# Kernel optimization log

Hardware: AMD Instinct MI355X
Metric: run time of the kernel (lower is better)

## Reference

```python
import jax, jax.numpy as jnp
import numpy as np

SEQ_LEN = 2048

def setup_inputs() -> dict:
    key = jax.random.key(0)
    kq, kk, kv = jax.random.split(key, 3)
    B, S, D = 8, SEQ_LEN, 64
    q = jax.random.normal(kq, (B, S, D), dtype=jnp.float32)
    k = jax.random.normal(kk, (B, S, D), dtype=jnp.float32)
    v = jax.random.normal(kv, (B, S, D), dtype=jnp.float32)
    return {"q": q, "k": k, "v": v}

def reference(q, k, v):
    # scores: [B, S, S] = q @ k^T  (note: original applies NO 1/sqrt(d) scaling)
    scores = jnp.einsum('bqd,bkd->bqk', q, k)
    S = scores.shape[-1]
    causal = jnp.tril(jnp.ones((S, S), dtype=bool))  # lower-triangular mask
    scores = jnp.where(causal, scores, -jnp.inf)
    weights = jax.nn.softmax(scores, axis=-1)
    return jnp.einsum('bqk,bkd->bqd', weights, v)
```

## Files before the change

kernel.cpp:

```cpp
#include <hip/hip_runtime.h>


#define BATCH 8
#define SEQ 2048
#define DIM 64
#define NEL (BATCH * SEQ * DIM)

typedef __attribute__((ext_vector_type(8))) short short8;
typedef __attribute__((ext_vector_type(4))) float f32x4;

#define MFMA(a, b, c) __builtin_amdgcn_mfma_f32_16x16x32_bf16(a, b, c, 0, 0, 0)

__device__ __forceinline__ unsigned short f2bf(float x) {
    unsigned u = __float_as_uint(x);
    unsigned r = u + 0x7fffu + ((u >> 16) & 1u);
    return (unsigned short)(r >> 16);
}
__device__ __forceinline__ float bf2f(unsigned short h) {
    return __uint_as_float(((unsigned)h) << 16);
}
__device__ __forceinline__ short8 ld8(const unsigned short* p) {
    return *(const short8*)p;
}
__device__ __forceinline__ void splitA(float4 a, float4 b, short8& h8, short8& l8) {
    float v[8] = {a.x, a.y, a.z, a.w, b.x, b.y, b.z, b.w};
#pragma unroll
    for (int i = 0; i < 8; ++i) {
        unsigned u  = __float_as_uint(v[i]);
        unsigned hu = u & 0xffff0000u;
        h8[i] = (short)(hu >> 16);
        float lf = v[i] - __uint_as_float(hu);
        l8[i] = (short)(__float_as_uint(lf) >> 16);
    }
}

__device__ __forceinline__ float dpp_max16(float x) {
    float o;
    o = __int_as_float(__builtin_amdgcn_update_dpp(0, __float_as_int(x), 0xB1, 0xF, 0xF, true));
    x = fmaxf(x, o);
    o = __int_as_float(__builtin_amdgcn_update_dpp(0, __float_as_int(x), 0x4E, 0xF, 0xF, true));
    x = fmaxf(x, o);
    o = __int_as_float(__builtin_amdgcn_update_dpp(0, __float_as_int(x), 0x141, 0xF, 0xF, true));
    x = fmaxf(x, o);
    o = __int_as_float(__builtin_amdgcn_update_dpp(0, __float_as_int(x), 0x140, 0xF, 0xF, true));
    return fmaxf(x, o);
}
__device__ __forceinline__ float dpp_sum16(float x) {
    float o;
    o = __int_as_float(__builtin_amdgcn_update_dpp(0, __float_as_int(x), 0xB1, 0xF, 0xF, true));
    x += o;
    o = __int_as_float(__builtin_amdgcn_update_dpp(0, __float_as_int(x), 0x4E, 0xF, 0xF, true));
    x += o;
    o = __int_as_float(__builtin_amdgcn_update_dpp(0, __float_as_int(x), 0x141, 0xF, 0xF, true));
    x += o;
    o = __int_as_float(__builtin_amdgcn_update_dpp(0, __float_as_int(x), 0x140, 0xF, 0xF, true));
    return x + o;
}

__global__ __launch_bounds__(256) void prep(
    const float* __restrict__ K, const float* __restrict__ V,
    unsigned short* __restrict__ Kf, unsigned short* __restrict__ Vf)
{
    __shared__ unsigned short sT[64][72];
    const int blk = blockIdx.x;
    const int t = threadIdx.x;

    if (blk < 512) {
        const int g  = blk * 256 + t;
        const int l  = g & 63;
        const int h  = (g >> 6) & 1;
        const int Sg = g >> 7;
        const int b  = Sg >> 7;
        const int S  = Sg & 127;
        const int key = S * 16 + (l & 15);
        const float* src = K + ((size_t)(b * SEQ + key)) * DIM + h * 32 + (l >> 4) * 8;
        float4 a = *(const float4*)src;
        float4 c = *(const float4*)(src + 4);
        float v[8] = {a.x, a.y, a.z, a.w, c.x, c.y, c.z, c.w};
        short8 h8, l8;
#pragma unroll
        for (int i = 0; i < 8; ++i) {
            unsigned short hh = f2bf(v[i]);
            h8[i] = (short)hh;
            l8[i] = (short)f2bf(v[i] - bf2f(hh));
        }
        unsigned short* dst = Kf + (((size_t)Sg) << 11) + (h << 9) + l * 8;
        *(short8*)dst = h8;
        *(short8*)(dst + 1024) = l8;
        return;
    }

    const int tile = blk - 512;
    const int b = tile >> 5;
    const int s0 = (tile & 31) * 64;
    const int srow = t >> 4;
    const int d4   = (t & 15) * 4;
#pragma unroll
    for (int i = 0; i < 4; ++i) {
        const int row = srow + i * 16;
        float4 v = *(const float4*)(V + ((size_t)(b * SEQ + s0 + row)) * DIM + d4);
        sT[d4 + 0][row] = f2bf(v.x);
        sT[d4 + 1][row] = f2bf(v.y);
        sT[d4 + 2][row] = f2bf(v.z);
        sT[d4 + 3][row] = f2bf(v.w);
    }
    __syncthreads();
#pragma unroll
    for (int i = 0; i < 2; ++i) {
        const int fid = t + i * 256;
        const int cc  = fid >> 8;
        const int nt  = (fid >> 6) & 3;
        const int l   = fid & 63;
        const int key = cc * 32 + (l >> 4) * 8;
        const int dim = nt * 16 + (l & 15);
        const int c   = (s0 >> 5) + cc;
        unsigned short* dst =
            Vf + ((((size_t)(b * 64 + c)) * 4 + nt) << 9) + l * 8;
        *(float4*)dst = *(const float4*)&sT[dim][key];
    }
}

__global__ __launch_bounds__(256) void attn_main(
    const float* __restrict__ Q,
    const unsigned short* __restrict__ Kf,
    const unsigned short* __restrict__ Vf, float* __restrict__ O)
{
    __shared__ __align__(16) char scratch[4][4352];
    __shared__ float sMl[4][16][2];

    const int bid  = blockIdx.x;
    const int g    = bid >> 8;
    const int idx  = bid & 255;
    const int b    = idx & (BATCH - 1);
    const int tl   = idx >> 3;
    const int qt   = (g & 1) ? (g * 32 + 31 - tl) : (g * 32 + tl);

    const int t    = threadIdx.x;
    const int w    = t >> 6;
    const int lane = t & 63;
    const int quad = lane >> 4;
    const int n16  = lane & 15;
    const int boff = b * SEQ;

    unsigned short* sPw = (unsigned short*)scratch[w];
    float*          sOw = (float*)scratch[w];

    const unsigned short* KfL = Kf + (((size_t)(b * 128)) << 11) + lane * 8;

    const int q0 = qt * 16;
    const int q_max = q0 + 15;

    short8 qh0, ql0, qh1, ql1;
    {
        const float* qb = Q + ((size_t)(boff + q0 + n16)) * DIM + quad * 8;
        splitA(*(const float4*)(qb),      *(const float4*)(qb + 4),  qh0, ql0);
        splitA(*(const float4*)(qb + 32), *(const float4*)(qb + 36), qh1, ql1);
    }

    float m0 = -1e30f, m1 = -1e30f, m2 = -1e30f, m3 = -1e30f;
    float l0 = 0.f, l1 = 0.f, l2 = 0.f, l3 = 0.f;
    f32x4 oacc[4];
#pragma unroll
    for (int i = 0; i < 4; ++i) oacc[i] = (f32x4){0.f, 0.f, 0.f, 0.f};

    for (int kb = w * 128; kb <= q_max; kb += 512) {
        const int rem  = q_max - kb;
        const int nsub = min(8, (rem >> 4) + 1);
        const int nchain = (nsub + 1) >> 1;
        f32x4 sacc[8];

#pragma unroll
        for (int gp = 0; gp < 4; ++gp) {
            const int stA = 2 * gp, stB = stA + 1;
            if (stA < nsub) {
                const unsigned short* pA = KfL + (((size_t)((kb >> 4) + stA)) << 11);
                short8 khA0 = ld8(pA),        khA1 = ld8(pA + 512);
                short8 klA0 = ld8(pA + 1024), klA1 = ld8(pA + 1536);
                const bool okB = (stB < nsub);
                const unsigned short* pB = KfL + (((size_t)((kb >> 4) + stB)) << 11);
                short8 khB0, khB1, klB0, klB1;
                if (okB) {
                    khB0 = ld8(pB);        khB1 = ld8(pB + 512);
                    klB0 = ld8(pB + 1024); klB1 = ld8(pB + 1536);
                }
                f32x4 accA = (f32x4){0.f, 0.f, 0.f, 0.f};
                accA = MFMA(qh0, khA0, accA);
                accA = MFMA(qh1, khA1, accA);
                accA = MFMA(qh0, klA0, accA);
                accA = MFMA(qh1, klA1, accA);
                accA = MFMA(ql0, khA0, accA);
                accA = MFMA(ql1, khA1, accA);
                sacc[stA] = accA;
                if (okB) {
                    f32x4 accB = (f32x4){0.f, 0.f, 0.f, 0.f};
                    accB = MFMA(qh0, khB0, accB);
                    accB = MFMA(qh1, khB1, accB);
                    accB = MFMA(qh0, klB0, accB);
                    accB = MFMA(qh1, klB1, accB);
                    accB = MFMA(ql0, khB0, accB);
                    accB = MFMA(ql1, khB1, accB);
                    sacc[stB] = accB;
                } else {
                    sacc[stB] = (f32x4){-1e30f, -1e30f, -1e30f, -1e30f};
                }
            } else {
                sacc[stA] = (f32x4){-1e30f, -1e30f, -1e30f, -1e30f};
                sacc[stB] = (f32x4){-1e30f, -1e30f, -1e30f, -1e30f};
            }
        }

        if (kb + 127 > q0) {
#pragma unroll
            for (int st = 0; st < 8; ++st) {
                if (st < nsub) {
                    const int key = kb + st * 16 + n16;
#pragma unroll
                    for (int r = 0; r < 4; ++r)
                        if (key > q0 + quad * 4 + r) sacc[st][r] = -1e30f;
                }
            }
        }

        float mt0 = sacc[0][0], mt1 = sacc[0][1], mt2 = sacc[0][2], mt3 = sacc[0][3];
#pragma unroll
        for (int st = 1; st < 8; ++st) {
            mt0 = fmaxf(mt0, sacc[st][0]);
            mt1 = fmaxf(mt1, sacc[st][1]);
            mt2 = fmaxf(mt2, sacc[st][2]);
            mt3 = fmaxf(mt3, sacc[st][3]);
        }
        mt0 = dpp_max16(mt0); mt1 = dpp_max16(mt1);
        mt2 = dpp_max16(mt2); mt3 = dpp_max16(mt3);
        const float mn0 = fmaxf(m0, mt0), mn1 = fmaxf(m1, mt1);
        const float mn2 = fmaxf(m2, mt2), mn3 = fmaxf(m3, mt3);
        const float a0 = __expf(m0 - mn0), a1 = __expf(m1 - mn1);
        const float a2 = __expf(m2 - mn2), a3 = __expf(m3 - mn3);
        m0 = mn0; m1 = mn1; m2 = mn2; m3 = mn3;

        float ps0 = 0.f, ps1 = 0.f, ps2 = 0.f, ps3 = 0.f;
        const int stmax = 2 * nchain;
#pragma unroll
        for (int st = 0; st < 8; ++st) {
            if (st < stmax) {
                float p0 = 0.f, p1 = 0.f, p2 = 0.f, p3 = 0.f;
                if (st < nsub) {
                    p0 = __expf(sacc[st][0] - mn0);
                    p1 = __expf(sacc[st][1] - mn1);
                    p2 = __expf(sacc[st][2] - mn2);
                    p3 = __expf(sacc[st][3] - mn3);
                    ps0 += p0; ps1 += p1; ps2 += p2; ps3 += p3;
                }
                const int col = st * 16 + n16;
                sPw[(quad * 4 + 0) * 136 + col] = f2bf(p0);
                sPw[(quad * 4 + 1) * 136 + col] = f2bf(p1);
                sPw[(quad * 4 + 2) * 136 + col] = f2bf(p2);
                sPw[(quad * 4 + 3) * 136 + col] = f2bf(p3);
            }
        }
        ps0 = dpp_sum16(ps0); ps1 = dpp_sum16(ps1);
        ps2 = dpp_sum16(ps2); ps3 = dpp_sum16(ps3);
        l0 = l0 * a0 + ps0; l1 = l1 * a1 + ps1;
        l2 = l2 * a2 + ps2; l3 = l3 * a3 + ps3;
#pragma unroll
        for (int nt = 0; nt < 4; ++nt) {
            oacc[nt][0] *= a0; oacc[nt][1] *= a1;
            oacc[nt][2] *= a2; oacc[nt][3] *= a3;
        }

#pragma unroll
        for (int ch = 0; ch < 4; ++ch) {
            if (ch < nchain) {
                short8 pa = ld8(&sPw[n16 * 136 + ch * 32 + quad * 8]);
                const size_t cbase =
                    (((size_t)(b * 64 + (kb >> 5) + ch)) * 4) << 9;
#pragma unroll
                for (int nt = 0; nt < 4; ++nt) {
                    short8 vv = ld8(Vf + cbase + (nt << 9) + lane * 8);
                    oacc[nt] = MFMA(pa, vv, oacc[nt]);
                }
            }
        }
    }

#pragma unroll
    for (int nt = 0; nt < 4; ++nt)
#pragma unroll
        for (int r = 0; r < 4; ++r)
            sOw[(quad * 4 + r) * 68 + nt * 16 + n16] = oacc[nt][r];
    if (n16 == 0) {
        sMl[w][quad * 4 + 0][0] = m0; sMl[w][quad * 4 + 0][1] = l0;
        sMl[w][quad * 4 + 1][0] = m1; sMl[w][quad * 4 + 1][1] = l1;
        sMl[w][quad * 4 + 2][0] = m2; sMl[w][quad * 4 + 2][1] = l2;
        sMl[w][quad * 4 + 3][0] = m3; sMl[w][quad * 4 + 3][1] = l3;
    }
    __syncthreads();

    const int row  = t >> 4;
    const int col4 = (t & 15) * 4;
    float M = fmaxf(fmaxf(sMl[0][row][0], sMl[1][row][0]),
                    fmaxf(sMl[2][row][0], sMl[3][row][0]));
    float L = 0.f;
    float ox = 0.f, oy = 0.f, oz = 0.f, ow = 0.f;
#pragma unroll
    for (int wv = 0; wv < 4; ++wv) {
        const float ew = __expf(sMl[wv][row][0] - M);
        L += ew * sMl[wv][row][1];
        const float* op = (const float*)scratch[wv] + row * 68 + col4;
        ox += ew * op[0]; oy += ew * op[1]; oz += ew * op[2]; ow += ew * op[3];
    }
    const float inv = 1.0f / L;
    float4 res = make_float4(ox * inv, oy * inv, oz * inv, ow * inv);
    *(float4*)(O + ((size_t)(boff + q0 + row)) * DIM + col4) = res;
}

extern "C" void kernel_launch(void* const* d_in, const int* in_sizes, int n_in,
                              void* d_out, int out_size, void* d_ws, size_t ws_size,
                              hipStream_t stream) {
    const float* q = (const float*)d_in[0];
    const float* k = (const float*)d_in[1];
    const float* v = (const float*)d_in[2];
    float* out = (float*)d_out;

    unsigned short* Kf = (unsigned short*)d_ws;
    unsigned short* Vf = Kf + 2 * NEL;

    prep<<<dim3(512 + 256), dim3(256), 0, stream>>>(k, v, Kf, Vf);
    attn_main<<<dim3(1024), dim3(256), 0, stream>>>(q, Kf, Vf, out);
}
```

Baseline: 90.27 us.

## Process 32 query rows per block to reuse K and V tiles across two query subtiles

Each block now handles 32 query rows as two 16-row subtiles that share every loaded K and V fragment, and the grid is halved to 512 blocks. This cuts global K/V load traffic per query row in half and amortises address math and the softmax bookkeeping loop. In exchange, register pressure roughly doubles (two sets of score and output accumulators), shared scratch doubles, and fewer blocks means less parallelism and coarser causal load balancing, even though the tile ordering is still paired front/back.

```diff
diff --git a/kernel.cpp b/kernel.cpp
--- a/kernel.cpp
+++ b/kernel.cpp
@@ -125,15 +125,15 @@
     const unsigned short* __restrict__ Kf,
     const unsigned short* __restrict__ Vf, float* __restrict__ O)
 {
-    __shared__ __align__(16) char scratch[4][4352];
-    __shared__ float sMl[4][16][2];
+    __shared__ __align__(16) char scratch[4][8704];
+    __shared__ float sMl[4][32][2];
 
     const int bid  = blockIdx.x;
-    const int g    = bid >> 8;
+    const int gph  = bid >> 8;
     const int idx  = bid & 255;
     const int b    = idx & (BATCH - 1);
     const int tl   = idx >> 3;
-    const int qt   = (g & 1) ? (g * 32 + 31 - tl) : (g * 32 + tl);
+    const int qt   = gph ? (63 - tl) : tl;
 
     const int t    = threadIdx.x;
     const int w    = t >> 6;
@@ -147,65 +147,60 @@
 
     const unsigned short* KfL = Kf + (((size_t)(b * 128)) << 11) + lane * 8;
 
-    const int q0 = qt * 16;
-    const int q_max = q0 + 15;
-
-    short8 qh0, ql0, qh1, ql1;
+    const int q0 = qt * 32;
+    const int q_max = q0 + 31;
+
+    short8 qAh0, qAl0, qAh1, qAl1, qBh0, qBl0, qBh1, qBl1;
     {
-        const float* qb = Q + ((size_t)(boff + q0 + n16)) * DIM + quad * 8;
-        splitA(*(const float4*)(qb),      *(const float4*)(qb + 4),  qh0, ql0);
-        splitA(*(const float4*)(qb + 32), *(const float4*)(qb + 36), qh1, ql1);
+        const float* qa = Q + ((size_t)(boff + q0 + n16)) * DIM + quad * 8;
+        splitA(*(const float4*)(qa),      *(const float4*)(qa + 4),  qAh0, qAl0);
+        splitA(*(const float4*)(qa + 32), *(const float4*)(qa + 36), qAh1, qAl1);
+        const float* qb = qa + 16 * DIM;
+        splitA(*(const float4*)(qb),      *(const float4*)(qb + 4),  qBh0, qBl0);
+        splitA(*(const float4*)(qb + 32), *(const float4*)(qb + 36), qBh1, qBl1);
     }
 
     float m0 = -1e30f, m1 = -1e30f, m2 = -1e30f, m3 = -1e30f;
+    float m4 = -1e30f, m5 = -1e30f, m6 = -1e30f, m7 = -1e30f;
     float l0 = 0.f, l1 = 0.f, l2 = 0.f, l3 = 0.f;
-    f32x4 oacc[4];
-#pragma unroll
-    for (int i = 0; i < 4; ++i) oacc[i] = (f32x4){0.f, 0.f, 0.f, 0.f};
+    float l4 = 0.f, l5 = 0.f, l6 = 0.f, l7 = 0.f;
+    f32x4 oacc0[4], oacc1[4];
+#pragma unroll
+    for (int i = 0; i < 4; ++i) {
+        oacc0[i] = (f32x4){0.f, 0.f, 0.f, 0.f};
+        oacc1[i] = (f32x4){0.f, 0.f, 0.f, 0.f};
+    }
 
     for (int kb = w * 128; kb <= q_max; kb += 512) {
-        const int rem  = q_max - kb;
-        const int nsub = min(8, (rem >> 4) + 1);
+        const int nsub = min(8, ((q_max - kb) >> 4) + 1);
         const int nchain = (nsub + 1) >> 1;
-        f32x4 sacc[8];
-
-#pragma unroll
-        for (int gp = 0; gp < 4; ++gp) {
-            const int stA = 2 * gp, stB = stA + 1;
-            if (stA < nsub) {
-                const unsigned short* pA = KfL + (((size_t)((kb >> 4) + stA)) << 11);
-                short8 khA0 = ld8(pA),        khA1 = ld8(pA + 512);
-                short8 klA0 = ld8(pA + 1024), klA1 = ld8(pA + 1536);
-                const bool okB = (stB < nsub);
-                const unsigned short* pB = KfL + (((size_t)((kb >> 4) + stB)) << 11);
-                short8 khB0, khB1, klB0, klB1;
-                if (okB) {
-                    khB0 = ld8(pB);        khB1 = ld8(pB + 512);
-                    klB0 = ld8(pB + 1024); klB1 = ld8(pB + 1536);
-                }
-                f32x4 accA = (f32x4){0.f, 0.f, 0.f, 0.f};
-                accA = MFMA(qh0, khA0, accA);
-                accA = MFMA(qh1, khA1, accA);
-                accA = MFMA(qh0, klA0, accA);
-                accA = MFMA(qh1, klA1, accA);
-                accA = MFMA(ql0, khA0, accA);
-                accA = MFMA(ql1, khA1, accA);
-                sacc[stA] = accA;
-                if (okB) {
-                    f32x4 accB = (f32x4){0.f, 0.f, 0.f, 0.f};
-                    accB = MFMA(qh0, khB0, accB);
-                    accB = MFMA(qh1, khB1, accB);
-                    accB = MFMA(qh0, klB0, accB);
-                    accB = MFMA(qh1, klB1, accB);
-                    accB = MFMA(ql0, khB0, accB);
-                    accB = MFMA(ql1, khB1, accB);
-                    sacc[stB] = accB;
-                } else {
-                    sacc[stB] = (f32x4){-1e30f, -1e30f, -1e30f, -1e30f};
-                }
+        f32x4 sacc0[8], sacc1[8];
+
+#pragma unroll
+        for (int st = 0; st < 8; ++st) {
+            if (st < nsub) {
+                const unsigned short* p = KfL + (((size_t)((kb >> 4) + st)) << 11);
+                short8 kh0 = ld8(p),        kh1 = ld8(p + 512);
+                short8 kl0 = ld8(p + 1024), kl1 = ld8(p + 1536);
+                f32x4 a = (f32x4){0.f, 0.f, 0.f, 0.f};
+                a = MFMA(qAh0, kh0, a);
+                a = MFMA(qAh1, kh1, a);
+                a = MFMA(qAh0, kl0, a);
+                a = MFMA(qAh1, kl1, a);
+                a = MFMA(qAl0, kh0, a);
+                a = MFMA(qAl1, kh1, a);
+                sacc0[st] = a;
+                f32x4 c = (f32x4){0.f, 0.f, 0.f, 0.f};
+                c = MFMA(qBh0, kh0, c);
+                c = MFMA(qBh1, kh1, c);
+                c = MFMA(qBh0, kl0, c);
+                c = MFMA(qBh1, kl1, c);
+                c = MFMA(qBl0, kh0, c);
+                c = MFMA(qBl1, kh1, c);
+                sacc1[st] = c;
             } else {
-                sacc[stA] = (f32x4){-1e30f, -1e30f, -1e30f, -1e30f};
-                sacc[stB] = (f32x4){-1e30f, -1e30f, -1e30f, -1e30f};
+                sacc0[st] = (f32x4){-1e30f, -1e30f, -1e30f, -1e30f};
+                sacc1[st] = (f32x4){-1e30f, -1e30f, -1e30f, -1e30f};
             }
         }
 
@@ -215,68 +210,101 @@
                 if (st < nsub) {
                     const int key = kb + st * 16 + n16;
 #pragma unroll
-                    for (int r = 0; r < 4; ++r)
-                        if (key > q0 + quad * 4 + r) sacc[st][r] = -1e30f;
+                    for (int r = 0; r < 4; ++r) {
+                        if (key > q0 + quad * 4 + r)      sacc0[st][r] = -1e30f;
+                        if (key > q0 + 16 + quad * 4 + r) sacc1[st][r] = -1e30f;
+                    }
                 }
             }
         }
 
-        float mt0 = sacc[0][0], mt1 = sacc[0][1], mt2 = sacc[0][2], mt3 = sacc[0][3];
+        float mt0 = sacc0[0][0], mt1 = sacc0[0][1], mt2 = sacc0[0][2], mt3 = sacc0[0][3];
+        float mt4 = sacc1[0][0], mt5 = sacc1[0][1], mt6 = sacc1[0][2], mt7 = sacc1[0][3];
 #pragma unroll
         for (int st = 1; st < 8; ++st) {
-            mt0 = fmaxf(mt0, sacc[st][0]);
-            mt1 = fmaxf(mt1, sacc[st][1]);
-            mt2 = fmaxf(mt2, sacc[st][2]);
-            mt3 = fmaxf(mt3, sacc[st][3]);
+            mt0 = fmaxf(mt0, sacc0[st][0]);
+            mt1 = fmaxf(mt1, sacc0[st][1]);
+            mt2 = fmaxf(mt2, sacc0[st][2]);
+            mt3 = fmaxf(mt3, sacc0[st][3]);
+            mt4 = fmaxf(mt4, sacc1[st][0]);
+            mt5 = fmaxf(mt5, sacc1[st][1]);
+            mt6 = fmaxf(mt6, sacc1[st][2]);
+            mt7 = fmaxf(mt7, sacc1[st][3]);
         }
         mt0 = dpp_max16(mt0); mt1 = dpp_max16(mt1);
         mt2 = dpp_max16(mt2); mt3 = dpp_max16(mt3);
+        mt4 = dpp_max16(mt4); mt5 = dpp_max16(mt5);
+        mt6 = dpp_max16(mt6); mt7 = dpp_max16(mt7);
         const float mn0 = fmaxf(m0, mt0), mn1 = fmaxf(m1, mt1);
         const float mn2 = fmaxf(m2, mt2), mn3 = fmaxf(m3, mt3);
+        const float mn4 = fmaxf(m4, mt4), mn5 = fmaxf(m5, mt5);
+        const float mn6 = fmaxf(m6, mt6), mn7 = fmaxf(m7, mt7);
         const float a0 = __expf(m0 - mn0), a1 = __expf(m1 - mn1);
         const float a2 = __expf(m2 - mn2), a3 = __expf(m3 - mn3);
+        const float a4 = __expf(m4 - mn4), a5 = __expf(m5 - mn5);
+        const float a6 = __expf(m6 - mn6), a7 = __expf(m7 - mn7);
         m0 = mn0; m1 = mn1; m2 = mn2; m3 = mn3;
+        m4 = mn4; m5 = mn5; m6 = mn6; m7 = mn7;
 
         float ps0 = 0.f, ps1 = 0.f, ps2 = 0.f, ps3 = 0.f;
+        float ps4 = 0.f, ps5 = 0.f, ps6 = 0.f, ps7 = 0.f;
         const int stmax = 2 * nchain;
 #pragma unroll
         for (int st = 0; st < 8; ++st) {
             if (st < stmax) {
                 float p0 = 0.f, p1 = 0.f, p2 = 0.f, p3 = 0.f;
+                float p4 = 0.f, p5 = 0.f, p6 = 0.f, p7 = 0.f;
                 if (st < nsub) {
-                    p0 = __expf(sacc[st][0] - mn0);
-                    p1 = __expf(sacc[st][1] - mn1);
-                    p2 = __expf(sacc[st][2] - mn2);
-                    p3 = __expf(sacc[st][3] - mn3);
+                    p0 = __expf(sacc0[st][0] - mn0);
+                    p1 = __expf(sacc0[st][1] - mn1);
+                    p2 = __expf(sacc0[st][2] - mn2);
+                    p3 = __expf(sacc0[st][3] - mn3);
+                    p4 = __expf(sacc1[st][0] - mn4);
+                    p5 = __expf(sacc1[st][1] - mn5);
+                    p6 = __expf(sacc1[st][2] - mn6);
+                    p7 = __expf(sacc1[st][3] - mn7);
                     ps0 += p0; ps1 += p1; ps2 += p2; ps3 += p3;
+                    ps4 += p4; ps5 += p5; ps6 += p6; ps7 += p7;
                 }
                 const int col = st * 16 + n16;
                 sPw[(quad * 4 + 0) * 136 + col] = f2bf(p0);
                 sPw[(quad * 4 + 1) * 136 + col] = f2bf(p1);
                 sPw[(quad * 4 + 2) * 136 + col] = f2bf(p2);
                 sPw[(quad * 4 + 3) * 136 + col] = f2bf(p3);
+                sPw[(16 + quad * 4 + 0) * 136 + col] = f2bf(p4);
+                sPw[(16 + quad * 4 + 1) * 136 + col] = f2bf(p5);
+                sPw[(16 + quad * 4 + 2) * 136 + col] = f2bf(p6);
+                sPw[(16 + quad * 4 + 3) * 136 + col] = f2bf(p7);
             }
         }
         ps0 = dpp_sum16(ps0); ps1 = dpp_sum16(ps1);
         ps2 = dpp_sum16(ps2); ps3 = dpp_sum16(ps3);
+        ps4 = dpp_sum16(ps4); ps5 = dpp_sum16(ps5);
+        ps6 = dpp_sum16(ps6); ps7 = dpp_sum16(ps7);
         l0 = l0 * a0 + ps0; l1 = l1 * a1 + ps1;
         l2 = l2 * a2 + ps2; l3 = l3 * a3 + ps3;
+        l4 = l4 * a4 + ps4; l5 = l5 * a5 + ps5;
+        l6 = l6 * a6 + ps6; l7 = l7 * a7 + ps7;
 #pragma unroll
         for (int nt = 0; nt < 4; ++nt) {
-            oacc[nt][0] *= a0; oacc[nt][1] *= a1;
-            oacc[nt][2] *= a2; oacc[nt][3] *= a3;
+            oacc0[nt][0] *= a0; oacc0[nt][1] *= a1;
+            oacc0[nt][2] *= a2; oacc0[nt][3] *= a3;
+            oacc1[nt][0] *= a4; oacc1[nt][1] *= a5;
+            oacc1[nt][2] *= a6; oacc1[nt][3] *= a7;
         }
 
 #pragma unroll
         for (int ch = 0; ch < 4; ++ch) {
             if (ch < nchain) {
-                short8 pa = ld8(&sPw[n16 * 136 + ch * 32 + quad * 8]);
+                short8 pa0 = ld8(&sPw[n16 * 136 + ch * 32 + quad * 8]);
+                short8 pa1 = ld8(&sPw[(16 + n16) * 136 + ch * 32 + quad * 8]);
                 const size_t cbase =
                     (((size_t)(b * 64 + (kb >> 5) + ch)) * 4) << 9;
 #pragma unroll
                 for (int nt = 0; nt < 4; ++nt) {
                     short8 vv = ld8(Vf + cbase + (nt << 9) + lane * 8);
-                    oacc[nt] = MFMA(pa, vv, oacc[nt]);
+                    oacc0[nt] = MFMA(pa0, vv, oacc0[nt]);
+                    oacc1[nt] = MFMA(pa1, vv, oacc1[nt]);
                 }
             }
         }
@@ -285,32 +313,43 @@
 #pragma unroll
     for (int nt = 0; nt < 4; ++nt)
 #pragma unroll
-        for (int r = 0; r < 4; ++r)
-            sOw[(quad * 4 + r) * 68 + nt * 16 + n16] = oacc[nt][r];
+        for (int r = 0; r < 4; ++r) {
+            sOw[(quad * 4 + r) * 68 + nt * 16 + n16]      = oacc0[nt][r];
+            sOw[(16 + quad * 4 + r) * 68 + nt * 16 + n16] = oacc1[nt][r];
+        }
     if (n16 == 0) {
         sMl[w][quad * 4 + 0][0] = m0; sMl[w][quad * 4 + 0][1] = l0;
         sMl[w][quad * 4 + 1][0] = m1; sMl[w][quad * 4 + 1][1] = l1;
         sMl[w][quad * 4 + 2][0] = m2; sMl[w][quad * 4 + 2][1] = l2;
         sMl[w][quad * 4 + 3][0] = m3; sMl[w][quad * 4 + 3][1] = l3;
+        sMl[w][16 + quad * 4 + 0][0] = m4; sMl[w][16 + quad * 4 + 0][1] = l4;
+        sMl[w][16 + quad * 4 + 1][0] = m5; sMl[w][16 + quad * 4 + 1][1] = l5;
+        sMl[w][16 + quad * 4 + 2][0] = m6; sMl[w][16 + quad * 4 + 2][1] = l6;
+        sMl[w][16 + quad * 4 + 3][0] = m7; sMl[w][16 + quad * 4 + 3][1] = l7;
     }
     __syncthreads();
 
-    const int row  = t >> 4;
-    const int col4 = (t & 15) * 4;
+    const int row  = t >> 3;
+    const int col8 = (t & 7) * 8;
     float M = fmaxf(fmaxf(sMl[0][row][0], sMl[1][row][0]),
                     fmaxf(sMl[2][row][0], sMl[3][row][0]));
     float L = 0.f;
-    float ox = 0.f, oy = 0.f, oz = 0.f, ow = 0.f;
+    float o0 = 0.f, o1 = 0.f, o2 = 0.f, o3 = 0.f;
+    float o4 = 0.f, o5 = 0.f, o6 = 0.f, o7 = 0.f;
 #pragma unroll
     for (int wv = 0; wv < 4; ++wv) {
         const float ew = __expf(sMl[wv][row][0] - M);
         L += ew * sMl[wv][row][1];
-        const float* op = (const float*)scratch[wv] + row * 68 + col4;
-        ox += ew * op[0]; oy += ew * op[1]; oz += ew * op[2]; ow += ew * op[3];
+        const float* op = (const float*)scratch[wv] + row * 68 + col8;
+        float4 va = *(const float4*)(op);
+        float4 vb = *(const float4*)(op + 4);
+        o0 += ew * va.x; o1 += ew * va.y; o2 += ew * va.z; o3 += ew * va.w;
+        o4 += ew * vb.x; o5 += ew * vb.y; o6 += ew * vb.z; o7 += ew * vb.w;
     }
     const float inv = 1.0f / L;
-    float4 res = make_float4(ox * inv, oy * inv, oz * inv, ow * inv);
-    *(float4*)(O + ((size_t)(boff + q0 + row)) * DIM + col4) = res;
+    float* dst = O + ((size_t)(boff + q0 + row)) * DIM + col8;
+    *(float4*)(dst)     = make_float4(o0 * inv, o1 * inv, o2 * inv, o3 * inv);
+    *(float4*)(dst + 4) = make_float4(o4 * inv, o5 * inv, o6 * inv, o7 * inv);
 }
 
 extern "C" void kernel_launch(void* const* d_in, const int* in_sizes, int n_in,
@@ -325,5 +364,5 @@
     unsigned short* Vf = Kf + 2 * NEL;
 
     prep<<<dim3(512 + 256), dim3(256), 0, stream>>>(k, v, Kf, Vf);
-    attn_main<<<dim3(1024), dim3(256), 0, stream>>>(q, Kf, Vf, out);
-}
+    attn_main<<<dim3(512), dim3(256), 0, stream>>>(q, Kf, Vf, out);
+}
```

After: 98.93 us. 1.1x slower.
